# Kernel tuning notes

Hardware: AMD Instinct MI355X
Metric: run time of the kernel (lower is better)

The kernel has to match this reference:

```python
import jax, jax.numpy as jnp
import numpy as np

V, H, NH, I, L, P = 32000, 1024, 16, 4096, 8, 2048
B, S = 2, 2048
DH = H // NH
EPS = 1e-5


def setup_inputs() -> dict:
    key = jax.random.key(0)
    ks = jax.random.split(key, 12)
    std = 0.02
    inp = {
        'input_ids': jax.random.randint(ks[0], (B, S), 0, V),
        'attention_mask': jnp.ones((B, S), dtype=jnp.float32),
        'tok_emb': jax.random.normal(ks[1], (V, H), jnp.float32) * std,
        'pos_emb': jax.random.normal(ks[2], (P, H), jnp.float32) * std,
        # per-layer params stacked on leading L dim (torch Linear convention: y = x @ W.T + b)
        'Wq': jax.random.normal(ks[3], (L, H, H), jnp.float32) * std,
        'bq': jnp.zeros((L, H), jnp.float32),
        'Wk': jax.random.normal(ks[4], (L, H, H), jnp.float32) * std,
        'bk': jnp.zeros((L, H), jnp.float32),
        'Wv': jax.random.normal(ks[5], (L, H, H), jnp.float32) * std,
        'bv': jnp.zeros((L, H), jnp.float32),
        'Wi': jax.random.normal(ks[6], (L, I, H), jnp.float32) * std,
        'bi': jnp.zeros((L, I), jnp.float32),
        'Wo': jax.random.normal(ks[7], (L, H, I), jnp.float32) * std,
        'bo': jnp.zeros((L, H), jnp.float32),
        'ln1_g': jnp.ones((L, H), jnp.float32),
        'ln1_b': jnp.zeros((L, H), jnp.float32),
        'ln2_g': jnp.ones((L, H), jnp.float32),
        'ln2_b': jnp.zeros((L, H), jnp.float32),
        'lnf_g': jnp.ones((H,), jnp.float32),
        'lnf_b': jnp.zeros((H,), jnp.float32),
        'Wlm': jax.random.normal(ks[8], (V, H), jnp.float32) * std,
    }
    return inp


def _layer_norm(x, g, b):
    m = jnp.mean(x, axis=-1, keepdims=True)
    v = jnp.var(x, axis=-1, keepdims=True)
    return (x - m) * jax.lax.rsqrt(v + EPS) * g + b


def reference(input_ids, attention_mask, tok_emb, pos_emb, Wq, bq, Wk, bk, Wv, bv,
              Wi, bi, Wo, bo, ln1_g, ln1_b, ln2_g, ln2_b, lnf_g, lnf_b, Wlm):
    b, s = input_ids.shape
    h = tok_emb[input_ids] + pos_emb[jnp.arange(s)][None, :, :]  # [B,S,H]
    mask = (1.0 - attention_mask)[:, None, None, :] * -10000.0   # [B,1,1,S]
    scale = 1.0 / (DH ** 0.5)

    def split_heads(x):  # [B,S,H] -> [B,NH,S,DH]
        return x.reshape(b, s, NH, DH).transpose(0, 2, 1, 3)

    def block(h, p):
        wq, bq_, wk, bk_, wv, bv_, wi, bi_, wo, bo_, g1, b1, g2, b2 = p
        q = split_heads(h @ wq.T + bq_)
        k = split_heads(h @ wk.T + bk_)
        v = split_heads(h @ wv.T + bv_)
        scores = jnp.einsum('bhqd,bhkd->bhqk', q, k) * scale + mask
        probs = jax.nn.softmax(scores, axis=-1)
        ctx = jnp.einsum('bhqk,bhkd->bhqd', probs, v)
        ctx = ctx.transpose(0, 2, 1, 3).reshape(b, s, H)
        h1 = _layer_norm(h + ctx, g1, b1)
        mlp = jax.nn.gelu(h1 @ wi.T + bi_, approximate=False) @ wo.T + bo_
        return _layer_norm(h1 + mlp, g2, b2), None

    h, _ = jax.lax.scan(block, h, (Wq, bq, Wk, bk, Wv, bv, Wi, bi, Wo, bo,
                                   ln1_g, ln1_b, ln2_g, ln2_b))
    h = _layer_norm(h, lnf_g, lnf_b)
    return h @ Wlm.T  # [B,S,V]
```

## Files before the change

### kernel.cpp

```cpp
#include <hip/hip_runtime.h>
#include <hip/hip_bf16.h>

#define V_ 32000
#define H_ 1024
#define NH_ 16
#define I_ 4096
#define L_ 8
#define B_ 2
#define S_ 2048
#define DH_ 64
#define M_ 4096
#define QS_ 3072

typedef __attribute__((ext_vector_type(4))) float f32x4;
typedef __attribute__((ext_vector_type(8))) short s16x8;

#define BARRIER() do { asm volatile("" ::: "memory"); __builtin_amdgcn_s_barrier(); asm volatile("" ::: "memory"); } while (0)
#define SCHEDB()  __builtin_amdgcn_sched_barrier(0)

__device__ __forceinline__ unsigned short f2b(float f) {
  union { float f; unsigned u; } x; x.f = f;
  return (unsigned short)((x.u + 0x7FFFu + ((x.u >> 16) & 1u)) >> 16);
}

__device__ __forceinline__ void gl_lds16(const unsigned short* g, unsigned short* l) {
  __builtin_amdgcn_global_load_lds(
      (__attribute__((address_space(1))) const void*)g,
      (__attribute__((address_space(3))) void*)l, 16, 0, 0);
}

__global__ __launch_bounds__(256) void wcvt(const float* __restrict__ src,
                                            unsigned short* __restrict__ dst) {
  size_t i = ((size_t)blockIdx.x * 256 + threadIdx.x) * 4;
  float4 v = *(const float4*)(src + i);
  ushort4 b;
  b.x = f2b(v.x); b.y = f2b(v.y); b.z = f2b(v.z); b.w = f2b(v.w);
  *(ushort4*)(dst + i) = b;
}

__global__ __launch_bounds__(256) void qkvcat_all(const float* __restrict__ q,
                                                  const float* __restrict__ k,
                                                  const float* __restrict__ v,
                                                  unsigned short* __restrict__ dst) {
  size_t i = ((size_t)blockIdx.x * 256 + threadIdx.x) * 4;
  size_t l = i / (3u * H_ * H_);
  size_t r = i - l * (3u * H_ * H_);
  const float* s; size_t off;
  if (r < (size_t)H_ * H_)          { s = q; off = l * H_ * H_ + r; }
  else if (r < 2u * H_ * H_)        { s = k; off = l * H_ * H_ + r - (size_t)H_ * H_; }
  else                              { s = v; off = l * H_ * H_ + r - 2u * H_ * H_; }
  float4 vv = *(const float4*)(s + off);
  ushort4 b;
  b.x = f2b(vv.x); b.y = f2b(vv.y); b.z = f2b(vv.z); b.w = f2b(vv.w);
  *(ushort4*)(dst + i) = b;
}

__global__ __launch_bounds__(256) void qkvcat(const float* __restrict__ q,
                                              const float* __restrict__ k,
                                              const float* __restrict__ v,
                                              unsigned short* __restrict__ dst) {
  int i = (blockIdx.x * 256 + threadIdx.x) * 4;
  const float* s; int off;
  if (i < H_ * H_)          { s = q; off = i; }
  else if (i < 2 * H_ * H_) { s = k; off = i - H_ * H_; }
  else                      { s = v; off = i - 2 * H_ * H_; }
  float4 vv = *(const float4*)(s + off);
  ushort4 b;
  b.x = f2b(vv.x); b.y = f2b(vv.y); b.z = f2b(vv.z); b.w = f2b(vv.w);
  *(ushort4*)(dst + i) = b;
}

__global__ __launch_bounds__(256) void bcat(const float* __restrict__ bq,
                                            const float* __restrict__ bk,
                                            const float* __restrict__ bv,
                                            float* __restrict__ dst) {
  int i = blockIdx.x * 256 + threadIdx.x;
  int l = i / (3 * H_), r = i - l * 3 * H_;
  int p = r >> 10, c = r & (H_ - 1);
  const float* s = (p == 0) ? bq : ((p == 1) ? bk : bv);
  dst[i] = s[l * H_ + c];
}

__global__ __launch_bounds__(256) void embed_kernel(
    const int* __restrict__ ids, const float* __restrict__ tok,
    const float* __restrict__ pos, float* __restrict__ h,
    unsigned short* __restrict__ xbf)
{
  int row = blockIdx.x;
  int c4 = threadIdx.x;
  int id = ids[row];
  int s = row & (S_ - 1);
  float4 tv = ((const float4*)(tok + (size_t)id * H_))[c4];
  float4 pv = ((const float4*)(pos + (size_t)s * H_))[c4];
  float4 v; v.x = tv.x + pv.x; v.y = tv.y + pv.y; v.z = tv.z + pv.z; v.w = tv.w + pv.w;
  ((float4*)(h + (size_t)row * H_))[c4] = v;
  ushort4 b; b.x = f2b(v.x); b.y = f2b(v.y); b.z = f2b(v.z); b.w = f2b(v.w);
  ((ushort4*)(xbf + (size_t)row * H_))[c4] = b;
}

template<int EPI>
__global__ __launch_bounds__(256) void gemm_bt(
    const unsigned short* __restrict__ A, const unsigned short* __restrict__ Wb,
    const float* __restrict__ bias, float* __restrict__ outf,
    unsigned short* __restrict__ outb, int M, int N, int K)
{
  __shared__ unsigned short As[128][32];
  __shared__ unsigned short Bs[128][32];
  int t = threadIdx.x;
  int lane = t & 63, wid = t >> 6;
  int m0 = blockIdx.x * 128, n0 = blockIdx.y * 128;
  int wm = (wid >> 1) * 64, wn = (wid & 1) * 64;
  int fr = lane & 15, kh = (lane >> 4) * 8;
  int lrow = lane >> 2, lcol = (lane & 3) * 8;

  f32x4 acc[4][4] = {};

  const unsigned short* Abase = A  + (size_t)(m0 + wid * 32 + lrow) * K + lcol;
  const unsigned short* Bbase = Wb + (size_t)(n0 + wid * 32 + lrow) * K + lcol;
  unsigned short* AL0 = &As[wid * 32][0];
  unsigned short* AL1 = &As[wid * 32 + 16][0];
  unsigned short* BL0 = &Bs[wid * 32][0];
  unsigned short* BL1 = &Bs[wid * 32 + 16][0];

  for (int k0 = 0; k0 < K; k0 += 32) {
    gl_lds16(Abase + k0,                     AL0);
    gl_lds16(Abase + k0 + (size_t)16 * K,    AL1);
    gl_lds16(Bbase + k0,                     BL0);
    gl_lds16(Bbase + k0 + (size_t)16 * K,    BL1);
    __syncthreads();
    s16x8 af[4], bfr[4];
    #pragma unroll
    for (int i = 0; i < 4; ++i) af[i]  = *(const s16x8*)(&As[wm + i * 16 + fr][kh]);
    #pragma unroll
    for (int j = 0; j < 4; ++j) bfr[j] = *(const s16x8*)(&Bs[wn + j * 16 + fr][kh]);
    #pragma unroll
    for (int i = 0; i < 4; ++i)
      #pragma unroll
      for (int j = 0; j < 4; ++j)
        acc[i][j] = __builtin_amdgcn_mfma_f32_16x16x32_bf16(af[i], bfr[j], acc[i][j], 0, 0, 0);
    __syncthreads();
  }

  int fq = lane >> 4;
  #pragma unroll
  for (int i = 0; i < 4; ++i) {
    #pragma unroll
    for (int j = 0; j < 4; ++j) {
      #pragma unroll
      for (int r = 0; r < 4; ++r) {
        int row = m0 + wm + i * 16 + fq * 4 + r;
        int col = n0 + wn + j * 16 + fr;
        float v = acc[i][j][r] + (bias ? bias[col] : 0.f);
        if (EPI == 0) {
          outf[(size_t)row * N + col] = v;
        } else if (EPI == 1) {
          float ge = 0.5f * v * (1.0f + erff(v * 0.70710678118f));
          outb[(size_t)row * N + col] = f2b(ge);
        } else {
          outb[(size_t)row * N + col] = f2b(v);
        }
      }
    }
  }
}

template<int EPI>
__global__ __launch_bounds__(512, 2) void gemm256(
    const unsigned short* __restrict__ A, const unsigned short* __restrict__ Wb,
    const float* __restrict__ bias, float* __restrict__ outf,
    unsigned short* __restrict__ outb, int M, int N, int K)
{
  __shared__ unsigned short ASm[2][16384];
  __shared__ unsigned short BSm[2][16384];

  const int t = threadIdx.x;
  const int lane = t & 63, wid = t >> 6;
  const int wm = wid >> 2, wn = wid & 3;
  const int fr = lane & 15, hi = lane >> 4;

  const int Nt = N >> 8;
  const int nwg = gridDim.x;
  const int cpx = nwg >> 3;
  int bid = (int)blockIdx.x;
  int swz = (bid & 7) * cpx + (bid >> 3);
  int band = swz / (4 * Nt);
  int rem = swz - band * (4 * Nt);
  const int m0 = (band * 4 + (rem & 3)) << 8;
  const int n0 = (rem >> 2) << 8;

  const int NT = K >> 6;

  const int srow = lane >> 3;
  const int scol = ((lane & 7) ^ srow) << 3;
  const int ch0 = wid * 2;

  const int axorb = (fr & 7) << 4;
  const int koe0 = ((hi * 16) ^ axorb) >> 1;
  const int koe1 = (((hi * 16) | 64) ^ axorb) >> 1;

  f32x4 acc[8][4] = {};

  auto stage_half = [&](int slot, int h, int k0) {
    if (h < 2) {
      const unsigned short* src =
          A + (size_t)(m0 + h * 128 + ch0 * 8 + srow) * K + k0 + scol;
      unsigned short* dst = &ASm[slot][(h * 128 + ch0 * 8) * 64];
      gl_lds16(src, dst);
      gl_lds16(src + (size_t)8 * K, dst + 8 * 64);
    } else {
      const unsigned short* src =
          Wb + (size_t)(n0 + (h - 2) * 128 + ch0 * 8 + srow) * K + k0 + scol;
      unsigned short* dst = &BSm[slot][((h - 2) * 128 + ch0 * 8) * 64];
      gl_lds16(src, dst);
      gl_lds16(src + (size_t)8 * K, dst + 8 * 64);
    }
  };

  stage_half(0, 2, 0); stage_half(0, 3, 0); stage_half(0, 0, 0); stage_half(0, 1, 0);

  s16x8 af0[4][2], af1[4][2], bfv[4][2];

  for (int T = 0; T < NT; ++T) {
    const int s = T & 1;
    const int k1 = (T + 1) << 6;
    const bool more = (T + 1 < NT);

    asm volatile("s_waitcnt vmcnt(0)" ::: "memory");
    BARRIER();

    const unsigned short* As_ = ASm[s];
    const unsigned short* Bs_ = BSm[s];

    #pragma unroll
    for (int mi = 0; mi < 4; ++mi) {
      const unsigned short* p = As_ + (wm * 128 + mi * 16 + fr) * 64;
      af0[mi][0] = *(const s16x8*)(p + koe0);
      af0[mi][1] = *(const s16x8*)(p + koe1);
    }
    #pragma unroll
    for (int nj = 0; nj < 4; ++nj) {
      const unsigned short* p = Bs_ + (wn * 64 + nj * 16 + fr) * 64;
      bfv[nj][0] = *(const s16x8*)(p + koe0);
      bfv[nj][1] = *(const s16x8*)(p + koe1);
    }
    if (more) stage_half(s ^ 1, 2, k1);
    SCHEDB();
    __builtin_amdgcn_s_setprio(1);
    #pragma unroll
    for (int mi = 0; mi < 4; ++mi)
      #pragma unroll
      for (int nj = 0; nj < 2; ++nj) {
        acc[mi][nj] = __builtin_amdgcn_mfma_f32_16x16x32_bf16(af0[mi][0], bfv[nj][0], acc[mi][nj], 0, 0, 0);
        acc[mi][nj] = __builtin_amdgcn_mfma_f32_16x16x32_bf16(af0[mi][1], bfv[nj][1], acc[mi][nj], 0, 0, 0);
      }
    __builtin_amdgcn_s_setprio(0);
    SCHEDB();

    #pragma unroll
    for (int mi = 0; mi < 4; ++mi) {
      const unsigned short* p = As_ + (wm * 128 + (mi + 4) * 16 + fr) * 64;
      af1[mi][0] = *(const s16x8*)(p + koe0);
      af1[mi][1] = *(const s16x8*)(p + koe1);
    }
    if (more) stage_half(s ^ 1, 3, k1);
    SCHEDB();
    __builtin_amdgcn_s_setprio(1);
    #pragma unroll
    for (int mi = 0; mi < 4; ++mi)
      #pragma unroll
      for (int nj = 2; nj < 4; ++nj) {
        acc[mi][nj] = __builtin_amdgcn_mfma_f32_16x16x32_bf16(af0[mi][0], bfv[nj][0], acc[mi][nj], 0, 0, 0);
        acc[mi][nj] = __builtin_amdgcn_mfma_f32_16x16x32_bf16(af0[mi][1], bfv[nj][1], acc[mi][nj], 0, 0, 0);
      }
    __builtin_amdgcn_s_setprio(0);
    SCHEDB();

    if (more) stage_half(s ^ 1, 0, k1);
    SCHEDB();
    __builtin_amdgcn_s_setprio(1);
    #pragma unroll
    for (int mi = 0; mi < 4; ++mi)
      #pragma unroll
      for (int nj = 2; nj < 4; ++nj) {
        acc[mi + 4][nj] = __builtin_amdgcn_mfma_f32_16x16x32_bf16(af1[mi][0], bfv[nj][0], acc[mi + 4][nj], 0, 0, 0);
        acc[mi + 4][nj] = __builtin_amdgcn_mfma_f32_16x16x32_bf16(af1[mi][1], bfv[nj][1], acc[mi + 4][nj], 0, 0, 0);
      }
    __builtin_amdgcn_s_setprio(0);
    SCHEDB();

    if (more) stage_half(s ^ 1, 1, k1);
    SCHEDB();
    __builtin_amdgcn_s_setprio(1);
    #pragma unroll
    for (int mi = 0; mi < 4; ++mi)
      #pragma unroll
      for (int nj = 0; nj < 2; ++nj) {
        acc[mi + 4][nj] = __builtin_amdgcn_mfma_f32_16x16x32_bf16(af1[mi][0], bfv[nj][0], acc[mi + 4][nj], 0, 0, 0);
        acc[mi + 4][nj] = __builtin_amdgcn_mfma_f32_16x16x32_bf16(af1[mi][1], bfv[nj][1], acc[mi + 4][nj], 0, 0, 0);
      }
    __builtin_amdgcn_s_setprio(0);
  }

  #pragma unroll
  for (int mi = 0; mi < 8; ++mi) {
    #pragma unroll
    for (int nj = 0; nj < 4; ++nj) {
      #pragma unroll
      for (int r = 0; r < 4; ++r) {
        int row = m0 + wm * 128 + mi * 16 + hi * 4 + r;
        int col = n0 + wn * 64 + nj * 16 + fr;
        float v = acc[mi][nj][r] + (bias ? bias[col] : 0.f);
        if (EPI == 0) {
          outf[(size_t)row * N + col] = v;
        } else if (EPI == 1) {
          float ge = 0.5f * v * (1.0f + erff(v * 0.70710678118f));
          outb[(size_t)row * N + col] = f2b(ge);
        } else {
          outb[(size_t)row * N + col] = f2b(v);
        }
      }
    }
  }
}

__global__ __launch_bounds__(256) void transpose_v_bf16(
    const unsigned short* __restrict__ v, unsigned short* __restrict__ vT)
{
  __shared__ unsigned short tile[32][34];
  int bh = blockIdx.z;
  int b = bh >> 4, hh = bh & 15;
  const unsigned short* src = v + (size_t)b * S_ * QS_ + hh * DH_;
  unsigned short* dst = vT + (size_t)bh * DH_ * S_;
  int s0 = blockIdx.x * 32, d0 = blockIdx.y * 32;
  int x = threadIdx.x, y = threadIdx.y;
  #pragma unroll
  for (int i = 0; i < 4; ++i)
    tile[y + i * 8][x] = src[(size_t)(s0 + y + i * 8) * QS_ + d0 + x];
  __syncthreads();
  #pragma unroll
  for (int i = 0; i < 4; ++i)
    dst[(size_t)(d0 + y + i * 8) * S_ + s0 + x] = tile[x][y + i * 8];
}

#define KB_ 64
__global__ __launch_bounds__(512) void flash_mfma(
    const unsigned short* __restrict__ qb,
    const unsigned short* __restrict__ kb,
    const unsigned short* __restrict__ vtb,
    const float* __restrict__ mask,
    float* __restrict__ ctx)
{
  __shared__ unsigned short K2[2][KB_ * DH_];
  __shared__ unsigned short V2[2][DH_ * KB_];
  __shared__ unsigned short Ps[8][16][72];
  __shared__ float xpose[8][16];

  const float LOG2E = 1.4426950408889634f;
  const float SCL = 0.125f * LOG2E;
  int t = threadIdx.x, lane = t & 63, wid = t >> 6;
  int blk = blockIdx.x;
  int bh = blk & 31, qt = blk >> 5;
  int b = bh >> 4, hh = bh & 15;
  int row0 = b * S_ + qt * 128 + wid * 16;
  int fr = lane & 15, hi = lane >> 4;
  const float* mrow = mask + (size_t)b * S_;

  s16x8 qf[2];
  {
    const unsigned short* qrow = qb + (size_t)(row0 + fr) * QS_ + hh * DH_;
    qf[0] = *(const s16x8*)(qrow + hi * 8);
    qf[1] = *(const s16x8*)(qrow + 32 + hi * 8);
  }

  float m_run = -3.0e38f, l_run = 0.f;
  f32x4 octx[4] = {};

  const unsigned short* Kbase = kb + (size_t)b * S_ * QS_ + hh * DH_;
  const unsigned short* Vbase = vtb + (size_t)bh * DH_ * S_;

  int crow = lane >> 3;
  int scol = ((lane & 7) ^ crow) * 8;

  auto stage = [&](int slot, int t0) {
    gl_lds16(Kbase + (size_t)(t0 + wid * 8 + crow) * QS_ + scol, &K2[slot][wid * 512]);
    gl_lds16(Vbase + (size_t)(wid * 8 + crow) * S_ + t0 + scol,  &V2[slot][wid * 512]);
  };

  stage(0, 0);

  const int swz = (fr & 7) * 8;

  for (int t0 = 0; t0 < S_; t0 += KB_) {
    int slot = (t0 >> 6) & 1;
    __syncthreads();
    if (t0 + KB_ < S_) stage(slot ^ 1, t0 + KB_);

    f32x4 sacc[4] = {};
    #pragma unroll
    for (int g = 0; g < 4; ++g) {
      #pragma unroll
      for (int i = 0; i < 2; ++i) {
        s16x8 kf = *(const s16x8*)(&K2[slot][(g * 16 + fr) * 64 + ((i * 32 + hi * 8) ^ swz)]);
        sacc[g] = __builtin_amdgcn_mfma_f32_16x16x32_bf16(kf, qf[i], sacc[g], 0, 0, 0);
      }
    }

    float sc[4][4];
    float tm = -3.0e38f;
    #pragma unroll
    for (int g = 0; g < 4; ++g) {
      float4 mq = *(const float4*)(mrow + t0 + g * 16 + hi * 4);
      #pragma unroll
      for (int r = 0; r < 4; ++r) {
        float mk = (1.0f - ((const float*)&mq)[r]) * (-10000.0f * LOG2E);
        float v = sacc[g][r] * SCL + mk;
        sc[g][r] = v;
        tm = fmaxf(tm, v);
      }
    }
    tm = fmaxf(tm, __shfl_xor(tm, 16));
    tm = fmaxf(tm, __shfl_xor(tm, 32));

    if (!__all(tm <= m_run + 8.0f)) {
      float mn = fmaxf(m_run, tm);
      float corr = exp2f(m_run - mn);
      m_run = mn; l_run *= corr;
      xpose[wid][fr] = corr;
      float cr0 = xpose[wid][hi * 4 + 0];
      float cr1 = xpose[wid][hi * 4 + 1];
      float cr2 = xpose[wid][hi * 4 + 2];
      float cr3 = xpose[wid][hi * 4 + 3];
      #pragma unroll
      for (int dg = 0; dg < 4; ++dg) {
        octx[dg][0] *= cr0; octx[dg][1] *= cr1;
        octx[dg][2] *= cr2; octx[dg][3] *= cr3;
      }
    }

    float ps = 0.f;
    #pragma unroll
    for (int g = 0; g < 4; ++g)
      #pragma unroll
      for (int r = 0; r < 4; ++r) {
        float p = exp2f(sc[g][r] - m_run);
        sc[g][r] = p;
        ps += p;
      }
    ps += __shfl_xor(ps, 16);
    ps += __shfl_xor(ps, 32);
    l_run += ps;

    #pragma unroll
    for (int g = 0; g < 4; ++g) {
      uint2 pk;
      pk.x = (unsigned)f2b(sc[g][0]) | ((unsigned)f2b(sc[g][1]) << 16);
      pk.y = (unsigned)f2b(sc[g][2]) | ((unsigned)f2b(sc[g][3]) << 16);
      *(uint2*)(&Ps[wid][fr][g * 16 + hi * 4]) = pk;
    }

    #pragma unroll
    for (int kc = 0; kc < 2; ++kc) {
      s16x8 pf = *(const s16x8*)(&Ps[wid][fr][kc * 32 + hi * 8]);
      #pragma unroll
      for (int dg = 0; dg < 4; ++dg) {
        s16x8 vf2 = *(const s16x8*)(&V2[slot][(dg * 16 + fr) * 64 + ((kc * 32 + hi * 8) ^ swz)]);
        octx[dg] = __builtin_amdgcn_mfma_f32_16x16x32_bf16(pf, vf2, octx[dg], 0, 0, 0);
      }
    }
  }

  xpose[wid][fr] = l_run;
  float i0 = 1.0f / xpose[wid][hi * 4 + 0];
  float i1 = 1.0f / xpose[wid][hi * 4 + 1];
  float i2 = 1.0f / xpose[wid][hi * 4 + 2];
  float i3 = 1.0f / xpose[wid][hi * 4 + 3];
  #pragma unroll
  for (int dg = 0; dg < 4; ++dg) {
    size_t base = (size_t)(row0 + hi * 4) * H_ + hh * DH_ + dg * 16 + fr;
    ctx[base]          = octx[dg][0] * i0;
    ctx[base + H_]     = octx[dg][1] * i1;
    ctx[base + 2 * H_] = octx[dg][2] * i2;
    ctx[base + 3 * H_] = octx[dg][3] * i3;
  }
}

__global__ __launch_bounds__(256) void add_ln(
    const float* __restrict__ x, const float* __restrict__ y,
    const float* __restrict__ g, const float* __restrict__ bb,
    float* __restrict__ outf, unsigned short* __restrict__ outb)
{
  __shared__ float a1[4], a2[4];
  int row = blockIdx.x, t = threadIdx.x;
  float4 v = ((const float4*)(x + (size_t)row * H_))[t];
  if (y) {
    float4 u = ((const float4*)(y + (size_t)row * H_))[t];
    v.x += u.x; v.y += u.y; v.z += u.z; v.w += u.w;
  }
  float s1 = v.x + v.y + v.z + v.w;
  float s2 = v.x * v.x + v.y * v.y + v.z * v.z + v.w * v.w;
  #pragma unroll
  for (int d = 32; d; d >>= 1) { s1 += __shfl_xor(s1, d); s2 += __shfl_xor(s2, d); }
  if ((t & 63) == 0) { a1[t >> 6] = s1; a2[t >> 6] = s2; }
  __syncthreads();
  s1 = a1[0] + a1[1] + a1[2] + a1[3];
  s2 = a2[0] + a2[1] + a2[2] + a2[3];
  float mean = s1 * (1.0f / H_);
  float var = s2 * (1.0f / H_) - mean * mean;
  float inv = rsqrtf(var + 1e-5f);
  float4 gv = ((const float4*)g)[t];
  float4 bv = ((const float4*)bb)[t];
  float4 o;
  o.x = (v.x - mean) * inv * gv.x + bv.x;
  o.y = (v.y - mean) * inv * gv.y + bv.y;
  o.z = (v.z - mean) * inv * gv.z + bv.z;
  o.w = (v.w - mean) * inv * gv.w + bv.w;
  if (outf) ((float4*)(outf + (size_t)row * H_))[t] = o;
  if (outb) {
    ushort4 ob; ob.x = f2b(o.x); ob.y = f2b(o.y); ob.z = f2b(o.z); ob.w = f2b(o.w);
    ((ushort4*)(outb + (size_t)row * H_))[t] = ob;
  }
}

extern "C" void kernel_launch(void* const* d_in, const int* in_sizes, int n_in,
                              void* d_out, int out_size, void* d_ws, size_t ws_size,
                              hipStream_t stream) {
  const int*   ids  = (const int*)d_in[0];
  const float* mask = (const float*)d_in[1];
  const float* tok  = (const float*)d_in[2];
  const float* pos  = (const float*)d_in[3];
  const float* Wq   = (const float*)d_in[4];
  const float* bq   = (const float*)d_in[5];
  const float* Wk   = (const float*)d_in[6];
  const float* bk   = (const float*)d_in[7];
  const float* Wv   = (const float*)d_in[8];
  const float* bv   = (const float*)d_in[9];
  const float* Wi   = (const float*)d_in[10];
  const float* bi   = (const float*)d_in[11];
  const float* Wo   = (const float*)d_in[12];
  const float* bo   = (const float*)d_in[13];
  const float* ln1g = (const float*)d_in[14];
  const float* ln1b = (const float*)d_in[15];
  const float* ln2g = (const float*)d_in[16];
  const float* ln2b = (const float*)d_in[17];
  const float* lnfg = (const float*)d_in[18];
  const float* lnfb = (const float*)d_in[19];
  const float* Wlm  = (const float*)d_in[20];
  float* out = (float*)d_out;

  char* w = (char*)d_ws;
  size_t off = 0;
  auto alloc = [&](size_t bytes) { void* p = w + off; off = (off + bytes + 255) & ~(size_t)255; return p; };
  float* h     = (float*)alloc((size_t)M_ * H_ * 4);
  float* ctxb  = (float*)alloc((size_t)M_ * H_ * 4);
  unsigned short* qkvb  = (unsigned short*)alloc((size_t)M_ * QS_ * 2);
  unsigned short* vtb   = (unsigned short*)alloc((size_t)B_ * NH_ * DH_ * S_ * 2);
  unsigned short* xbf   = (unsigned short*)alloc((size_t)M_ * H_ * 2);
  unsigned short* midbf = (unsigned short*)alloc((size_t)M_ * I_ * 2);
  float* bqkv  = (float*)alloc((size_t)L_ * QS_ * 4);

  size_t wqkv_b = (size_t)L_ * 3 * H_ * H_ * 2;
  size_t wi_bb  = (size_t)L_ * I_ * H_ * 2;
  size_t wo_bb  = (size_t)L_ * H_ * I_ * 2;
  size_t wlm_bb = (size_t)V_ * H_ * 2;
  bool big = (ws_size - off) >= (wqkv_b + wi_bb + wo_bb + wlm_bb + 4 * 256);

  unsigned short *wqkv, *wi_a, *wo_a, *wlm_a, *wbuf = nullptr;
  if (big) {
    wqkv  = (unsigned short*)alloc(wqkv_b);
    wi_a  = (unsigned short*)alloc(wi_bb);
    wo_a  = (unsigned short*)alloc(wo_bb);
    wlm_a = (unsigned short*)alloc(wlm_bb);
    qkvcat_all<<<dim3((unsigned)((size_t)L_ * 3 * H_ * H_ / 1024)), 256, 0, stream>>>(Wq, Wk, Wv, wqkv);
    wcvt<<<dim3((unsigned)((size_t)L_ * I_ * H_ / 1024)), 256, 0, stream>>>(Wi, wi_a);
    wcvt<<<dim3((unsigned)((size_t)L_ * H_ * I_ / 1024)), 256, 0, stream>>>(Wo, wo_a);
    wcvt<<<dim3((unsigned)((size_t)V_ * H_ / 1024)), 256, 0, stream>>>(Wlm, wlm_a);
  } else {
    wbuf = (unsigned short*)alloc((size_t)V_ * H_ * 2);
  }

  bcat<<<dim3(L_ * QS_ / 256), 256, 0, stream>>>(bq, bk, bv, bqkv);
  embed_kernel<<<dim3(M_), 256, 0, stream>>>(ids, tok, pos, h, xbf);

  for (int l = 0; l < L_; ++l) {
    const unsigned short* wq_l;
    if (big) wq_l = wqkv + (size_t)l * 3 * H_ * H_;
    else {
      qkvcat<<<dim3(3 * H_ * H_ / 1024), 256, 0, stream>>>(
          Wq + (size_t)l * H_ * H_, Wk + (size_t)l * H_ * H_, Wv + (size_t)l * H_ * H_, wbuf);
      wq_l = wbuf;
    }
    gemm_bt<2><<<dim3(M_ / 128, QS_ / 128), 256, 0, stream>>>(
        xbf, wq_l, bqkv + (size_t)l * QS_, nullptr, qkvb, M_, QS_, H_);

    transpose_v_bf16<<<dim3(S_ / 32, DH_ / 32, B_ * NH_), dim3(32, 8), 0, stream>>>(
        qkvb + 2 * H_, vtb);
    flash_mfma<<<dim3(B_ * NH_ * S_ / 128), 512, 0, stream>>>(
        qkvb, qkvb + H_, vtb, mask, ctxb);

    add_ln<<<dim3(M_), 256, 0, stream>>>(h, ctxb, ln1g + l * H_, ln1b + l * H_, h, xbf);

    const unsigned short* wi_l;
    if (big) wi_l = wi_a + (size_t)l * I_ * H_;
    else {
      wcvt<<<dim3(I_ * H_ / 1024), 256, 0, stream>>>(Wi + (size_t)l * I_ * H_, wbuf);
      wi_l = wbuf;
    }
    gemm256<1><<<dim3((M_ / 256) * (I_ / 256)), 512, 0, stream>>>(
        xbf, wi_l, bi + l * I_, nullptr, midbf, M_, I_, H_);

    const unsigned short* wo_l;
    if (big) wo_l = wo_a + (size_t)l * H_ * I_;
    else {
      wcvt<<<dim3(H_ * I_ / 1024), 256, 0, stream>>>(Wo + (size_t)l * H_ * I_, wbuf);
      wo_l = wbuf;
    }
    gemm_bt<0><<<dim3(M_ / 128, H_ / 128), 256, 0, stream>>>(
        midbf, wo_l, bo + l * H_, ctxb, nullptr, M_, H_, I_);

    add_ln<<<dim3(M_), 256, 0, stream>>>(h, ctxb, ln2g + l * H_, ln2b + l * H_, h, xbf);
  }

  add_ln<<<dim3(M_), 256, 0, stream>>>(h, nullptr, lnfg, lnfb, nullptr, xbf);
  const unsigned short* wlm_l;
  if (big) wlm_l = wlm_a;
  else {
    wcvt<<<dim3(V_ * H_ / 1024), 256, 0, stream>>>(Wlm, wbuf);
    wlm_l = wbuf;
  }
  gemm256<0><<<dim3((M_ / 256) * (V_ / 256)), 512, 0, stream>>>(
      xbf, wlm_l, nullptr, out, nullptr, M_, V_, H_);
}
```

Measured before the change: 3.255 ms.

## Double-buffer gemm_bt with swizzled LDS, hoist gemm256 prefetch, split-KV flash attention

gemm_bt now double-buffers its LDS tiles with an XOR swizzle and prefetches the next K tile right after the barrier, which drops one barrier per iteration and reduces bank conflicts. gemm256 issues all next-tile staging loads at the top of the iteration instead of spreading them between MFMA groups. Flash attention splits the KV range into two halves across twice as many blocks, writing unnormalized partial outputs plus per-row max and sum. A new merge kernel then combines the two partials. This raises parallelism for attention, at the cost of extra fp32 partial-output traffic and one more launch.

```diff
diff --git a/kernel.cpp b/kernel.cpp
--- a/kernel.cpp
+++ b/kernel.cpp
@@ -104,41 +104,48 @@
     const float* __restrict__ bias, float* __restrict__ outf,
     unsigned short* __restrict__ outb, int M, int N, int K)
 {
-  __shared__ unsigned short As[128][32];
-  __shared__ unsigned short Bs[128][32];
+  __shared__ unsigned short As[2][128][32];
+  __shared__ unsigned short Bs[2][128][32];
   int t = threadIdx.x;
   int lane = t & 63, wid = t >> 6;
   int m0 = blockIdx.x * 128, n0 = blockIdx.y * 128;
   int wm = (wid >> 1) * 64, wn = (wid & 1) * 64;
-  int fr = lane & 15, kh = (lane >> 4) * 8;
-  int lrow = lane >> 2, lcol = (lane & 3) * 8;
+  int fr = lane & 15, hi = lane >> 4;
+  int lrow = lane >> 2;
+  int lcolsw = (((lane & 3) ^ (lrow & 3)) * 8);
+  int ke = ((hi ^ (fr & 3)) * 8);
 
   f32x4 acc[4][4] = {};
 
-  const unsigned short* Abase = A  + (size_t)(m0 + wid * 32 + lrow) * K + lcol;
-  const unsigned short* Bbase = Wb + (size_t)(n0 + wid * 32 + lrow) * K + lcol;
-  unsigned short* AL0 = &As[wid * 32][0];
-  unsigned short* AL1 = &As[wid * 32 + 16][0];
-  unsigned short* BL0 = &Bs[wid * 32][0];
-  unsigned short* BL1 = &Bs[wid * 32 + 16][0];
-
+  const unsigned short* Abase = A  + (size_t)(m0 + wid * 32 + lrow) * K + lcolsw;
+  const unsigned short* Bbase = Wb + (size_t)(n0 + wid * 32 + lrow) * K + lcolsw;
+
+  auto stage = [&](int s, int k0) {
+    gl_lds16(Abase + k0,                  &As[s][wid * 32][0]);
+    gl_lds16(Abase + k0 + (size_t)16 * K, &As[s][wid * 32 + 16][0]);
+    gl_lds16(Bbase + k0,                  &Bs[s][wid * 32][0]);
+    gl_lds16(Bbase + k0 + (size_t)16 * K, &Bs[s][wid * 32 + 16][0]);
+  };
+
+  stage(0, 0);
+
+  int cur = 0;
   for (int k0 = 0; k0 < K; k0 += 32) {
-    gl_lds16(Abase + k0,                     AL0);
-    gl_lds16(Abase + k0 + (size_t)16 * K,    AL1);
-    gl_lds16(Bbase + k0,                     BL0);
-    gl_lds16(Bbase + k0 + (size_t)16 * K,    BL1);
-    __syncthreads();
+    asm volatile("s_waitcnt vmcnt(0)" ::: "memory");
+    BARRIER();
+    if (k0 + 32 < K) stage(cur ^ 1, k0 + 32);
+    SCHEDB();
     s16x8 af[4], bfr[4];
     #pragma unroll
-    for (int i = 0; i < 4; ++i) af[i]  = *(const s16x8*)(&As[wm + i * 16 + fr][kh]);
-    #pragma unroll
-    for (int j = 0; j < 4; ++j) bfr[j] = *(const s16x8*)(&Bs[wn + j * 16 + fr][kh]);
+    for (int i = 0; i < 4; ++i) af[i]  = *(const s16x8*)(&As[cur][wm + i * 16 + fr][ke]);
+    #pragma unroll
+    for (int j = 0; j < 4; ++j) bfr[j] = *(const s16x8*)(&Bs[cur][wn + j * 16 + fr][ke]);
     #pragma unroll
     for (int i = 0; i < 4; ++i)
       #pragma unroll
       for (int j = 0; j < 4; ++j)
         acc[i][j] = __builtin_amdgcn_mfma_f32_16x16x32_bf16(af[i], bfr[j], acc[i][j], 0, 0, 0);
-    __syncthreads();
+    cur ^= 1;
   }
 
   int fq = lane >> 4;
@@ -227,6 +234,11 @@
 
     asm volatile("s_waitcnt vmcnt(0)" ::: "memory");
     BARRIER();
+    if (more) {
+      stage_half(s ^ 1, 2, k1); stage_half(s ^ 1, 3, k1);
+      stage_half(s ^ 1, 0, k1); stage_half(s ^ 1, 1, k1);
+    }
+    SCHEDB();
 
     const unsigned short* As_ = ASm[s];
     const unsigned short* Bs_ = BSm[s];
@@ -243,7 +255,6 @@
       bfv[nj][0] = *(const s16x8*)(p + koe0);
       bfv[nj][1] = *(const s16x8*)(p + koe1);
     }
-    if (more) stage_half(s ^ 1, 2, k1);
     SCHEDB();
     __builtin_amdgcn_s_setprio(1);
     #pragma unroll
@@ -262,7 +273,6 @@
       af1[mi][0] = *(const s16x8*)(p + koe0);
       af1[mi][1] = *(const s16x8*)(p + koe1);
     }
-    if (more) stage_half(s ^ 1, 3, k1);
     SCHEDB();
     __builtin_amdgcn_s_setprio(1);
     #pragma unroll
@@ -275,8 +285,6 @@
     __builtin_amdgcn_s_setprio(0);
     SCHEDB();
 
-    if (more) stage_half(s ^ 1, 0, k1);
-    SCHEDB();
     __builtin_amdgcn_s_setprio(1);
     #pragma unroll
     for (int mi = 0; mi < 4; ++mi)
@@ -288,8 +296,6 @@
     __builtin_amdgcn_s_setprio(0);
     SCHEDB();
 
-    if (more) stage_half(s ^ 1, 1, k1);
-    SCHEDB();
     __builtin_amdgcn_s_setprio(1);
     #pragma unroll
     for (int mi = 0; mi < 4; ++mi)
@@ -343,12 +349,14 @@
 }
 
 #define KB_ 64
+#define SPL_ 1024
 __global__ __launch_bounds__(512) void flash_mfma(
     const unsigned short* __restrict__ qb,
     const unsigned short* __restrict__ kb,
     const unsigned short* __restrict__ vtb,
     const float* __restrict__ mask,
-    float* __restrict__ ctx)
+    float* __restrict__ opart,
+    float2* __restrict__ ml)
 {
   __shared__ unsigned short K2[2][KB_ * DH_];
   __shared__ unsigned short V2[2][DH_ * KB_];
@@ -359,11 +367,14 @@
   const float SCL = 0.125f * LOG2E;
   int t = threadIdx.x, lane = t & 63, wid = t >> 6;
   int blk = blockIdx.x;
-  int bh = blk & 31, qt = blk >> 5;
+  int bh = blk & 31;
+  int rest = blk >> 5;
+  int qt = rest & 15, sp = rest >> 4;
   int b = bh >> 4, hh = bh & 15;
   int row0 = b * S_ + qt * 128 + wid * 16;
   int fr = lane & 15, hi = lane >> 4;
   const float* mrow = mask + (size_t)b * S_;
+  const int kv0 = sp * SPL_;
 
   s16x8 qf[2];
   {
@@ -386,14 +397,15 @@
     gl_lds16(Vbase + (size_t)(wid * 8 + crow) * S_ + t0 + scol,  &V2[slot][wid * 512]);
   };
 
-  stage(0, 0);
+  stage(0, kv0);
 
   const int swz = (fr & 7) * 8;
 
-  for (int t0 = 0; t0 < S_; t0 += KB_) {
-    int slot = (t0 >> 6) & 1;
+  int tt = 0;
+  for (int t0 = kv0; t0 < kv0 + SPL_; t0 += KB_, ++tt) {
+    int slot = tt & 1;
     __syncthreads();
-    if (t0 + KB_ < S_) stage(slot ^ 1, t0 + KB_);
+    if (t0 + KB_ < kv0 + SPL_) stage(slot ^ 1, t0 + KB_);
 
     f32x4 sacc[4] = {};
     #pragma unroll
@@ -469,19 +481,41 @@
     }
   }
 
-  xpose[wid][fr] = l_run;
-  float i0 = 1.0f / xpose[wid][hi * 4 + 0];
-  float i1 = 1.0f / xpose[wid][hi * 4 + 1];
-  float i2 = 1.0f / xpose[wid][hi * 4 + 2];
-  float i3 = 1.0f / xpose[wid][hi * 4 + 3];
+  float* ob = opart + (size_t)sp * M_ * H_;
   #pragma unroll
   for (int dg = 0; dg < 4; ++dg) {
     size_t base = (size_t)(row0 + hi * 4) * H_ + hh * DH_ + dg * 16 + fr;
-    ctx[base]          = octx[dg][0] * i0;
-    ctx[base + H_]     = octx[dg][1] * i1;
-    ctx[base + 2 * H_] = octx[dg][2] * i2;
-    ctx[base + 3 * H_] = octx[dg][3] * i3;
-  }
+    ob[base]          = octx[dg][0];
+    ob[base + H_]     = octx[dg][1];
+    ob[base + 2 * H_] = octx[dg][2];
+    ob[base + 3 * H_] = octx[dg][3];
+  }
+  if (hi == 0)
+    ml[((size_t)sp * 32 + bh) * S_ + qt * 128 + wid * 16 + fr] =
+        make_float2(m_run, l_run);
+}
+
+__global__ __launch_bounds__(256) void flash_merge(
+    const float* __restrict__ o0, const float* __restrict__ o1,
+    const float2* __restrict__ ml, float* __restrict__ ctx)
+{
+  int row = blockIdx.x, t = threadIdx.x;
+  int hh = t >> 4;
+  int bh = (row >> 11) * NH_ + hh;
+  int q = row & (S_ - 1);
+  float2 a = ml[(size_t)bh * S_ + q];
+  float2 c = ml[(size_t)(32 + bh) * S_ + q];
+  float m = fmaxf(a.x, c.x);
+  float w0 = exp2f(a.x - m), w1 = exp2f(c.x - m);
+  float inv = 1.0f / (a.y * w0 + c.y * w1);
+  float4 v0 = ((const float4*)(o0 + (size_t)row * H_))[t];
+  float4 v1 = ((const float4*)(o1 + (size_t)row * H_))[t];
+  float4 o;
+  o.x = (v0.x * w0 + v1.x * w1) * inv;
+  o.y = (v0.y * w0 + v1.y * w1) * inv;
+  o.z = (v0.z * w0 + v1.z * w1) * inv;
+  o.w = (v0.w * w0 + v1.w * w1) * inv;
+  ((float4*)(ctx + (size_t)row * H_))[t] = o;
 }
 
 __global__ __launch_bounds__(256) void add_ln(
@@ -557,6 +591,8 @@
   unsigned short* xbf   = (unsigned short*)alloc((size_t)M_ * H_ * 2);
   unsigned short* midbf = (unsigned short*)alloc((size_t)M_ * I_ * 2);
   float* bqkv  = (float*)alloc((size_t)L_ * QS_ * 4);
+  float* opart = (float*)alloc((size_t)2 * M_ * H_ * 4);
+  float2* mlbuf = (float2*)alloc((size_t)2 * 32 * S_ * 8);
 
   size_t wqkv_b = (size_t)L_ * 3 * H_ * H_ * 2;
   size_t wi_bb  = (size_t)L_ * I_ * H_ * 2;
@@ -594,8 +630,10 @@
 
     transpose_v_bf16<<<dim3(S_ / 32, DH_ / 32, B_ * NH_), dim3(32, 8), 0, stream>>>(
         qkvb + 2 * H_, vtb);
-    flash_mfma<<<dim3(B_ * NH_ * S_ / 128), 512, 0, stream>>>(
-        qkvb, qkvb + H_, vtb, mask, ctxb);
+    flash_mfma<<<dim3(B_ * NH_ * S_ / 128 * 2), 512, 0, stream>>>(
+        qkvb, qkvb + H_, vtb, mask, opart, mlbuf);
+    flash_merge<<<dim3(M_), 256, 0, stream>>>(
+        opart, opart + (size_t)M_ * H_, mlbuf, ctxb);
 
     add_ln<<<dim3(M_), 256, 0, stream>>>(h, ctxb, ln1g + l * H_, ln1b + l * H_, h, xbf);
 
```

After: 3.267 ms. No clear change (+0.4%).
